# Optimization experiments

Hardware: AMD Instinct MI355X
Metric: run time of the kernel (lower is better)

Reference implementation:

```python
import jax, jax.numpy as jnp
import numpy as np
from jax import lax


def _shifted(X, k, alpha):
    # alpha * roll(X, -k, 0) + (1 - alpha) * roll(X, -k-1, 0), via gather
    N = X.shape[0]
    idx = (jnp.arange(N) + k) % N
    return alpha * X[idx] + (1.0 - alpha) * X[(idx + 1) % N]


def _all_distances(D_q, D_p, steps):
    # steps: [S] float32 signed step values. Returns [S] mean L2 distances.
    N = D_q.shape[0]
    rows = jnp.arange(N)

    def dist_one(step):
        s = jnp.abs(step)
        k = jnp.floor(s).astype(jnp.int32)          # int(step) of |step|
        alpha = s - k.astype(step.dtype)
        diff = lax.cond(
            step >= 0,
            lambda: _shifted(D_q, k, alpha) - D_p,   # shift query forward
            lambda: D_q - _shifted(D_p, k, alpha),   # shift positive (ref) forward
        )
        norms = jnp.sqrt(jnp.sum(diff * diff, axis=-1))  # [N]
        valid = rows < (N - k)                       # rows [:N - int_step]
        return jnp.sum(jnp.where(valid, norms, 0.0)) / (N - k).astype(norms.dtype)

    def body(carry, step):
        return carry, dist_one(step)

    _, dists = lax.scan(body, None, steps)
    return dists


def setup_inputs() -> dict:
    key = jax.random.key(0)
    k1, k2 = jax.random.split(key)
    N, D = 100000, 256
    return {
        "D_q": jax.random.normal(k1, (N, D), dtype=jnp.float32),
        "D_p": jax.random.normal(k2, (N, D), dtype=jnp.float32),
        "max_step": 60,
        "step_size": 1,
    }


def reference(D_q, D_p, max_step, step_size):
    # Same candidate step schedule as the torch loop (static, built on host).
    steps_np = np.concatenate([
        np.arange(0, max_step, step_size),
        -np.arange(1, max_step + 1, step_size),
    ]).astype(np.float32)
    steps = jnp.asarray(steps_np)                    # [2*max_step/step_size]
    dists = _all_distances(D_q, D_p, steps)
    i = jnp.argmin(dists)
    return steps[i], dists[i]
```

## Files before the change

### kernel.cpp

```cpp
#include <hip/hip_runtime.h>
#include <math.h>


typedef __attribute__((ext_vector_type(8))) __bf16 bf16x8;
typedef __attribute__((ext_vector_type(4))) float f32x4;
typedef __attribute__((ext_vector_type(8))) unsigned short us8;

#define LDB 264
#define RING 10
#define MAXS 128
#define NREP 32

__global__ __launch_bounds__(576, 1)
void band_kernel(const float* __restrict__ Q, const float* __restrict__ P,
                 double* __restrict__ ws,
                 const int* __restrict__ msp, const int* __restrict__ ssp,
                 int N, int TS, int nsb) {
  __shared__ unsigned short Bsh[RING * 16 * LDB];
  __shared__ unsigned short Qsh[2 * 16 * LDB];
  __shared__ float NpS[RING * 16];
  __shared__ float NqS[2 * 16];
  __shared__ float sums[MAXS];

  const int t = threadIdx.x;
  const int ms = msp[0], ss = ssp[0];
  const int S1 = (ms + ss - 1) / ss;
  const int S = 2 * S1;

  const int T0 = blockIdx.x * nsb;
  int ns = TS - T0; if (ns > nsb) ns = nsb;
  if (ns <= 0) return;

  for (int i = t; i < MAXS; i += 576) sums[i] = 0.f;

  const int srow = t >> 5;
  const int scol = (t & 31) * 8;
  const bool stg = (t < 512);

  auto issue = [&](const float* __restrict__ base, int tau, float4& r0, float4& r1) {
    const int gr = tau * 16 + srow;
    if (stg && gr >= 0 && gr < N) {
      const float* s = base + (size_t)gr * 256 + scol;
      r0 = *reinterpret_cast<const float4*>(s);
      r1 = *reinterpret_cast<const float4*>(s + 4);
    } else {
      r0 = make_float4(0.f, 0.f, 0.f, 0.f);
      r1 = make_float4(0.f, 0.f, 0.f, 0.f);
    }
  };

  auto commit = [&](unsigned short* dst, float* ndst, int slot, float4 r0, float4 r1) {
    if (!stg) return;
    const float f[8] = {r0.x, r0.y, r0.z, r0.w, r1.x, r1.y, r1.z, r1.w};
    us8 h;
    float nrm = 0.f;
    #pragma unroll
    for (int j = 0; j < 8; ++j) {
      nrm = fmaf(f[j], f[j], nrm);
      h[j] = __builtin_bit_cast(unsigned short, (__bf16)f[j]);
    }
    *reinterpret_cast<us8*>(&dst[slot * 16 * LDB + srow * LDB + scol]) = h;
    #pragma unroll
    for (int m = 16; m >= 1; m >>= 1) nrm += __shfl_xor(nrm, m, 64);
    if ((t & 31) == 0) ndst[slot * 16 + srow] = nrm;
  };

  const int lane = t & 63;
  const int wid = t >> 6;
  const int l15 = lane & 15;
  const int kg = lane >> 4;

  int slotR[4];
  {
    const int base = 64 - 16 * wid + 4 * kg;
    #pragma unroll
    for (int r = 0; r < 4; ++r) {
      const int d = base + r - l15;
      int slot = -1;
      if (d >= 1) {
        const int k = d - 1;
        if (k < ms && (k % ss) == 0) slot = k / ss;
      } else if (d <= -2) {
        const int kk = -d - 1;
        if (kk <= ms && ((kk - 1) % ss) == 0) slot = S1 + (kk - 1) / ss;
      }
      if (slot >= MAXS) slot = -1;
      slotR[r] = slot;
    }
  }
  float racc[4] = {0.f, 0.f, 0.f, 0.f};

  float4 qA0, qA1, pA0, pA1, qB0, qB1, pB0, pB1;
  {
    float4 q0, q1, a0, a1, b0, b1, c0, c1;
    issue(Q, T0, q0, q1);
    issue(P, T0 - 4, a0, a1);
    issue(P, T0 - 3, b0, b1);
    issue(P, T0 - 2, c0, c1);
    #pragma unroll 1
    for (int i = 0; i < 9; ++i) {
      commit(Bsh, NpS, (T0 - 4 + i + 40) % RING, a0, a1);
      a0 = b0; a1 = b1; b0 = c0; b1 = c1;
      if (i < 6) issue(P, T0 - 1 + i, c0, c1);
    }
    commit(Qsh, NqS, T0 & 1, q0, q1);
    issue(Q, T0 + 1, qA0, qA1);
    issue(P, T0 + 5, pA0, pA1);
  }
  __syncthreads();

  #pragma unroll 1
  for (int s = 0; s < ns; ++s) {
    const int T = T0 + s;
    issue(Q, T + 2, qB0, qB1);
    issue(P, T + 6, pB0, pB1);

    const int tauW = T - 4 + wid;
    const int slotW = (tauW + 40) % RING;
    const unsigned short* Ab = &Qsh[(T & 1) * 16 * LDB + l15 * LDB + kg * 8];
    const unsigned short* Bb = &Bsh[slotW * 16 * LDB + l15 * LDB + kg * 8];
    f32x4 acc0 = {0.f, 0.f, 0.f, 0.f};
    f32x4 acc1 = {0.f, 0.f, 0.f, 0.f};
    #pragma unroll
    for (int ks = 0; ks < 8; ks += 2) {
      const bf16x8 av0 = *reinterpret_cast<const bf16x8*>(Ab + ks * 32);
      const bf16x8 bv0 = *reinterpret_cast<const bf16x8*>(Bb + ks * 32);
      const bf16x8 av1 = *reinterpret_cast<const bf16x8*>(Ab + ks * 32 + 32);
      const bf16x8 bv1 = *reinterpret_cast<const bf16x8*>(Bb + ks * 32 + 32);
      acc0 = __builtin_amdgcn_mfma_f32_16x16x32_bf16(av0, bv0, acc0, 0, 0, 0);
      acc1 = __builtin_amdgcn_mfma_f32_16x16x32_bf16(av1, bv1, acc1, 0, 0, 0);
    }

    const int bb = tauW * 16 + l15;
    if (bb >= 0 && bb < N) {
      const float npW = NpS[slotW * 16 + l15];
      const int as16 = T * 16 + kg * 4;
      #pragma unroll
      for (int r = 0; r < 4; ++r) {
        if (slotR[r] >= 0 && (as16 + r) < N) {
          const float n2 = NqS[(T & 1) * 16 + kg * 4 + r] + npW
                           - 2.0f * (acc0[r] + acc1[r]);
          racc[r] += sqrtf(fmaxf(n2, 0.f));
        }
      }
    }

    commit(Qsh, NqS, (T + 1) & 1, qA0, qA1);
    commit(Bsh, NpS, (T + 5 + 40) % RING, pA0, pA1);
    qA0 = qB0; qA1 = qB1; pA0 = pB0; pA1 = pB1;
    __syncthreads();
  }

  #pragma unroll
  for (int r = 0; r < 4; ++r)
    if (slotR[r] >= 0 && racc[r] != 0.f) atomicAdd(&sums[slotR[r]], racc[r]);
  __syncthreads();

  if (t < S && t < MAXS) {
    const float v = sums[t];
    if (v != 0.f)
      unsafeAtomicAdd(&ws[(size_t)(blockIdx.x & (NREP - 1)) * MAXS + t], (double)v);
  }
}

__global__ void corner_kernel(const float* __restrict__ Q, const float* __restrict__ P,
                              double* __restrict__ ws,
                              const int* __restrict__ msp, const int* __restrict__ ssp,
                              int N) {
  const int ms = msp[0], ss = ssp[0];
  const int S1 = (ms + ss - 1) / ss;
  const int S = 2 * S1;
  const int s = blockIdx.x;
  if (s >= S) return;
  int k, qr, pr;
  if (s < S1) { k = s * ss;            qr = 0;           pr = N - (k + 1); }
  else        { k = 1 + (s - S1) * ss; qr = N - (k + 1); pr = 0; }
  const int t = threadIdx.x;
  const float e = Q[(size_t)qr * 256 + t] - P[(size_t)pr * 256 + t];
  float sq = e * e;
  #pragma unroll
  for (int off = 32; off >= 1; off >>= 1) sq += __shfl_down(sq, off);
  __shared__ float red[4];
  if ((t & 63) == 0) red[t >> 6] = sq;
  __syncthreads();
  if (t == 0)
    ws[(size_t)NREP * MAXS + s] = (double)sqrtf(red[0] + red[1] + red[2] + red[3]);
}

__global__ void finalize_kernel(const double* __restrict__ ws, float* __restrict__ out,
                                const int* __restrict__ msp, const int* __restrict__ ssp,
                                int N) {
  __shared__ double dist_sh[MAXS];
  const int t = threadIdx.x;
  const int ms = msp[0], ss = ssp[0];
  const int S1 = (ms + ss - 1) / ss;
  const int S = 2 * S1;
  if (t < S && t < MAXS) {
    double tot = 0.0;
    for (int rep = 0; rep < NREP; ++rep) tot += ws[(size_t)rep * MAXS + t];
    tot += ws[(size_t)NREP * MAXS + t];
    const int k = (t < S1) ? t * ss : 1 + (t - S1) * ss;
    dist_sh[t] = tot / (double)(N - k);
  }
  __syncthreads();
  if (t == 0) {
    int best = 0;
    double bd = dist_sh[0];
    for (int s = 1; s < S && s < MAXS; ++s)
      if (dist_sh[s] < bd) { bd = dist_sh[s]; best = s; }
    const int k = (best < S1) ? best * ss : 1 + (best - S1) * ss;
    out[0] = (best < S1) ? (float)k : -(float)k;
    out[1] = (float)bd;
  }
}

extern "C" void kernel_launch(void* const* d_in, const int* in_sizes, int n_in,
                              void* d_out, int out_size, void* d_ws, size_t ws_size,
                              hipStream_t stream) {
  const float* Q   = (const float*)d_in[0];
  const float* P   = (const float*)d_in[1];
  const int*   msp = (const int*)d_in[2];
  const int*   ssp = (const int*)d_in[3];
  const int N = in_sizes[0] / 256;
  double* ws = (double*)d_ws;

  hipMemsetAsync(d_ws, 0, (size_t)(NREP + 1) * MAXS * sizeof(double), stream);

  const int TS = (N + 15) / 16;
  int nsb = (TS + 255) / 256;
  if (nsb < 1) nsb = 1;
  const int grid = (TS + nsb - 1) / nsb;

  band_kernel<<<grid, 576, 0, stream>>>(Q, P, ws, msp, ssp, N, TS, nsb);
  corner_kernel<<<MAXS, 256, 0, stream>>>(Q, P, ws, msp, ssp, N);
  finalize_kernel<<<1, 128, 0, stream>>>(ws, (float*)d_out, msp, ssp, N);
}
```

Baseline: 70.88 us.

## Switch band kernel to 32-row tiles with 32x32x16 MFMA and smaller ring

Moves the band-diagonal distance computation from 16x16 MFMA tiles with nine compute waves to 32x32x16 MFMA tiles with five compute waves covering a 5-tile band. Staging now uses 512 threads loading 32 rows per step, and the grid is resized to about 250 blocks. The aim is to cut per-step overhead and redundant computation outside the band relative to useful diagonals, and to halve the step count. The trade-off is more accumulator registers (16 per lane, two sets), three idle waves during compute, and larger LDS tiles.

```diff
diff --git a/kernel.cpp b/kernel.cpp
--- a/kernel.cpp
+++ b/kernel.cpp
@@ -3,23 +3,22 @@
 
 
 typedef __attribute__((ext_vector_type(8))) __bf16 bf16x8;
-typedef __attribute__((ext_vector_type(4))) float f32x4;
-typedef __attribute__((ext_vector_type(8))) unsigned short us8;
-
-#define LDB 264
-#define RING 10
+typedef __attribute__((ext_vector_type(16))) float f32x16;
+
+#define LDSH 280
+#define RING 6
 #define MAXS 128
 #define NREP 32
 
-__global__ __launch_bounds__(576, 1)
+__global__ __launch_bounds__(512, 1)
 void band_kernel(const float* __restrict__ Q, const float* __restrict__ P,
                  double* __restrict__ ws,
                  const int* __restrict__ msp, const int* __restrict__ ssp,
                  int N, int TS, int nsb) {
-  __shared__ unsigned short Bsh[RING * 16 * LDB];
-  __shared__ unsigned short Qsh[2 * 16 * LDB];
-  __shared__ float NpS[RING * 16];
-  __shared__ float NqS[2 * 16];
+  __shared__ __align__(16) unsigned short Bsh[RING * 32 * LDSH];
+  __shared__ __align__(16) unsigned short Qsh[2 * 32 * LDSH];
+  __shared__ float NpS[RING * 32];
+  __shared__ float NqS[2 * 32];
   __shared__ float sums[MAXS];
 
   const int t = threadIdx.x;
@@ -31,52 +30,56 @@
   int ns = TS - T0; if (ns > nsb) ns = nsb;
   if (ns <= 0) return;
 
-  for (int i = t; i < MAXS; i += 576) sums[i] = 0.f;
-
-  const int srow = t >> 5;
-  const int scol = (t & 31) * 8;
-  const bool stg = (t < 512);
-
-  auto issue = [&](const float* __restrict__ base, int tau, float4& r0, float4& r1) {
-    const int gr = tau * 16 + srow;
-    if (stg && gr >= 0 && gr < N) {
-      const float* s = base + (size_t)gr * 256 + scol;
-      r0 = *reinterpret_cast<const float4*>(s);
-      r1 = *reinterpret_cast<const float4*>(s + 4);
+  for (int i = t; i < MAXS; i += 512) sums[i] = 0.f;
+
+  const int srow = t >> 4;
+  const int sc = (t & 15) * 4;
+
+  auto issue = [&](const float* __restrict__ base, int tau, float4* r) {
+    const int gr = tau * 32 + srow;
+    if (gr >= 0 && gr < N) {
+      const float* s = base + (size_t)gr * 256 + sc;
+      #pragma unroll
+      for (int j = 0; j < 4; ++j)
+        r[j] = *reinterpret_cast<const float4*>(s + j * 64);
     } else {
-      r0 = make_float4(0.f, 0.f, 0.f, 0.f);
-      r1 = make_float4(0.f, 0.f, 0.f, 0.f);
+      #pragma unroll
+      for (int j = 0; j < 4; ++j) r[j] = make_float4(0.f, 0.f, 0.f, 0.f);
     }
   };
 
-  auto commit = [&](unsigned short* dst, float* ndst, int slot, float4 r0, float4 r1) {
-    if (!stg) return;
-    const float f[8] = {r0.x, r0.y, r0.z, r0.w, r1.x, r1.y, r1.z, r1.w};
-    us8 h;
+  auto commit = [&](unsigned short* dst, float* ndst, int slot, const float4* r) {
     float nrm = 0.f;
+    unsigned short* row = dst + slot * 32 * LDSH + srow * LDSH;
     #pragma unroll
-    for (int j = 0; j < 8; ++j) {
-      nrm = fmaf(f[j], f[j], nrm);
-      h[j] = __builtin_bit_cast(unsigned short, (__bf16)f[j]);
-    }
-    *reinterpret_cast<us8*>(&dst[slot * 16 * LDB + srow * LDB + scol]) = h;
-    #pragma unroll
-    for (int m = 16; m >= 1; m >>= 1) nrm += __shfl_xor(nrm, m, 64);
-    if ((t & 31) == 0) ndst[slot * 16 + srow] = nrm;
+    for (int j = 0; j < 4; ++j) {
+      const float f0 = r[j].x, f1 = r[j].y, f2 = r[j].z, f3 = r[j].w;
+      nrm = fmaf(f0, f0, nrm); nrm = fmaf(f1, f1, nrm);
+      nrm = fmaf(f2, f2, nrm); nrm = fmaf(f3, f3, nrm);
+      ushort4 h;
+      h.x = __builtin_bit_cast(unsigned short, (__bf16)f0);
+      h.y = __builtin_bit_cast(unsigned short, (__bf16)f1);
+      h.z = __builtin_bit_cast(unsigned short, (__bf16)f2);
+      h.w = __builtin_bit_cast(unsigned short, (__bf16)f3);
+      *reinterpret_cast<ushort4*>(row + j * 64 + sc) = h;
+    }
+    nrm += __shfl_xor(nrm, 1); nrm += __shfl_xor(nrm, 2);
+    nrm += __shfl_xor(nrm, 4); nrm += __shfl_xor(nrm, 8);
+    if ((t & 15) == 0) ndst[slot * 32 + srow] = nrm;
   };
 
   const int lane = t & 63;
   const int wid = t >> 6;
-  const int l15 = lane & 15;
-  const int kg = lane >> 4;
-
-  int slotR[4];
-  {
-    const int base = 64 - 16 * wid + 4 * kg;
-    #pragma unroll
-    for (int r = 0; r < 4; ++r) {
-      const int d = base + r - l15;
-      int slot = -1;
+  const int l31 = lane & 31;
+  const int hi = lane >> 5;
+
+  int slotR[16];
+  #pragma unroll
+  for (int r = 0; r < 16; ++r) {
+    int slot = -1;
+    if (wid < 5) {
+      const int arow = (r & 3) + 8 * (r >> 2) + 4 * hi;
+      const int d = arow - l31 - (wid - 2) * 32;
       if (d >= 1) {
         const int k = d - 1;
         if (k < ms && (k % ss) == 0) slot = k / ss;
@@ -85,74 +88,78 @@
         if (kk <= ms && ((kk - 1) % ss) == 0) slot = S1 + (kk - 1) / ss;
       }
       if (slot >= MAXS) slot = -1;
-      slotR[r] = slot;
-    }
-  }
-  float racc[4] = {0.f, 0.f, 0.f, 0.f};
-
-  float4 qA0, qA1, pA0, pA1, qB0, qB1, pB0, pB1;
+    }
+    slotR[r] = slot;
+  }
+  float racc[16];
+  #pragma unroll
+  for (int r = 0; r < 16; ++r) racc[r] = 0.f;
+
+  float4 qA[4], pA[4], qB[4], pB[4];
   {
-    float4 q0, q1, a0, a1, b0, b1, c0, c1;
-    issue(Q, T0, q0, q1);
-    issue(P, T0 - 4, a0, a1);
-    issue(P, T0 - 3, b0, b1);
-    issue(P, T0 - 2, c0, c1);
-    #pragma unroll 1
-    for (int i = 0; i < 9; ++i) {
-      commit(Bsh, NpS, (T0 - 4 + i + 40) % RING, a0, a1);
-      a0 = b0; a1 = b1; b0 = c0; b1 = c1;
-      if (i < 6) issue(P, T0 - 1 + i, c0, c1);
-    }
-    commit(Qsh, NqS, T0 & 1, q0, q1);
-    issue(Q, T0 + 1, qA0, qA1);
-    issue(P, T0 + 5, pA0, pA1);
+    float4 u[4], v[4];
+    issue(P, T0 - 2, u);
+    #pragma unroll
+    for (int i = 0; i < 5; ++i) {
+      if (i < 4) issue(P, T0 - 1 + i, v);
+      commit(Bsh, NpS, (T0 - 2 + i + 12) % RING, u);
+      #pragma unroll
+      for (int j = 0; j < 4; ++j) u[j] = v[j];
+    }
+    issue(Q, T0, u);
+    commit(Qsh, NqS, T0 & 1, u);
+    issue(Q, T0 + 1, qA);
+    issue(P, T0 + 3, pA);
   }
   __syncthreads();
 
   #pragma unroll 1
   for (int s = 0; s < ns; ++s) {
     const int T = T0 + s;
-    issue(Q, T + 2, qB0, qB1);
-    issue(P, T + 6, pB0, pB1);
-
-    const int tauW = T - 4 + wid;
-    const int slotW = (tauW + 40) % RING;
-    const unsigned short* Ab = &Qsh[(T & 1) * 16 * LDB + l15 * LDB + kg * 8];
-    const unsigned short* Bb = &Bsh[slotW * 16 * LDB + l15 * LDB + kg * 8];
-    f32x4 acc0 = {0.f, 0.f, 0.f, 0.f};
-    f32x4 acc1 = {0.f, 0.f, 0.f, 0.f};
-    #pragma unroll
-    for (int ks = 0; ks < 8; ks += 2) {
-      const bf16x8 av0 = *reinterpret_cast<const bf16x8*>(Ab + ks * 32);
-      const bf16x8 bv0 = *reinterpret_cast<const bf16x8*>(Bb + ks * 32);
-      const bf16x8 av1 = *reinterpret_cast<const bf16x8*>(Ab + ks * 32 + 32);
-      const bf16x8 bv1 = *reinterpret_cast<const bf16x8*>(Bb + ks * 32 + 32);
-      acc0 = __builtin_amdgcn_mfma_f32_16x16x32_bf16(av0, bv0, acc0, 0, 0, 0);
-      acc1 = __builtin_amdgcn_mfma_f32_16x16x32_bf16(av1, bv1, acc1, 0, 0, 0);
-    }
-
-    const int bb = tauW * 16 + l15;
-    if (bb >= 0 && bb < N) {
-      const float npW = NpS[slotW * 16 + l15];
-      const int as16 = T * 16 + kg * 4;
-      #pragma unroll
-      for (int r = 0; r < 4; ++r) {
-        if (slotR[r] >= 0 && (as16 + r) < N) {
-          const float n2 = NqS[(T & 1) * 16 + kg * 4 + r] + npW
-                           - 2.0f * (acc0[r] + acc1[r]);
-          racc[r] += sqrtf(fmaxf(n2, 0.f));
+    issue(Q, T + 2, qB);
+    issue(P, T + 4, pB);
+
+    if (wid < 5) {
+      const int tauW = T - 2 + wid;
+      const int slot6 = (tauW + 12) % RING;
+      const unsigned short* Ab = &Qsh[(T & 1) * 32 * LDSH + l31 * LDSH + hi * 8];
+      const unsigned short* Bb = &Bsh[slot6 * 32 * LDSH + l31 * LDSH + hi * 8];
+      f32x16 acc0 = {}, acc1 = {};
+      #pragma unroll
+      for (int ks = 0; ks < 16; ks += 2) {
+        const bf16x8 a0 = *reinterpret_cast<const bf16x8*>(Ab + ks * 16);
+        const bf16x8 b0 = *reinterpret_cast<const bf16x8*>(Bb + ks * 16);
+        const bf16x8 a1 = *reinterpret_cast<const bf16x8*>(Ab + ks * 16 + 16);
+        const bf16x8 b1 = *reinterpret_cast<const bf16x8*>(Bb + ks * 16 + 16);
+        acc0 = __builtin_amdgcn_mfma_f32_32x32x16_bf16(a0, b0, acc0, 0, 0, 0);
+        acc1 = __builtin_amdgcn_mfma_f32_32x32x16_bf16(a1, b1, acc1, 0, 0, 0);
+      }
+
+      const int bcol = tauW * 32 + l31;
+      if (bcol >= 0 && bcol < N) {
+        const float npW = NpS[slot6 * 32 + l31];
+        const int aT = T * 32;
+        #pragma unroll
+        for (int r = 0; r < 16; ++r) {
+          const int arow = (r & 3) + 8 * (r >> 2) + 4 * hi;
+          if (slotR[r] >= 0 && (aT + arow) < N) {
+            const float n2 = NqS[(T & 1) * 32 + arow] + npW
+                             - 2.0f * (acc0[r] + acc1[r]);
+            racc[r] += sqrtf(fmaxf(n2, 0.f));
+          }
         }
       }
     }
 
-    commit(Qsh, NqS, (T + 1) & 1, qA0, qA1);
-    commit(Bsh, NpS, (T + 5 + 40) % RING, pA0, pA1);
-    qA0 = qB0; qA1 = qB1; pA0 = pB0; pA1 = pB1;
+    commit(Qsh, NqS, (T + 1) & 1, qA);
+    commit(Bsh, NpS, (T + 3 + 12) % RING, pA);
+    #pragma unroll
+    for (int j = 0; j < 4; ++j) { qA[j] = qB[j]; pA[j] = pB[j]; }
     __syncthreads();
   }
 
   #pragma unroll
-  for (int r = 0; r < 4; ++r)
+  for (int r = 0; r < 16; ++r)
     if (slotR[r] >= 0 && racc[r] != 0.f) atomicAdd(&sums[slotR[r]], racc[r]);
   __syncthreads();
 
@@ -226,12 +233,12 @@
 
   hipMemsetAsync(d_ws, 0, (size_t)(NREP + 1) * MAXS * sizeof(double), stream);
 
-  const int TS = (N + 15) / 16;
-  int nsb = (TS + 255) / 256;
+  const int TS = (N + 31) / 32;
+  int nsb = (TS + 249) / 250;
   if (nsb < 1) nsb = 1;
   const int grid = (TS + nsb - 1) / nsb;
 
-  band_kernel<<<grid, 576, 0, stream>>>(Q, P, ws, msp, ssp, N, TS, nsb);
+  band_kernel<<<grid, 512, 0, stream>>>(Q, P, ws, msp, ssp, N, TS, nsb);
   corner_kernel<<<MAXS, 256, 0, stream>>>(Q, P, ws, msp, ssp, N);
   finalize_kernel<<<1, 128, 0, stream>>>(ws, (float*)d_out, msp, ssp, N);
 }
```

New measurement: 74.31 us. 1.05x slower.
